# Kernel tuning notes

Measured on AMD Instinct MI355X. Metric: run time of the kernel, lower is better.

## Reference

```python
import jax, jax.numpy as jnp
import numpy as np

B, S, T, F, C = 32, 8, 1024, 128, 1
CLIP = 10.0

def setup_inputs() -> dict:
    key = jax.random.key(0)
    k1, k2 = jax.random.split(key)
    specs = jax.random.normal(k1, (B, S, T, F, C), dtype=jnp.float32)
    mask = jax.random.randint(k2, (B, S), 0, 2, dtype=jnp.int32)
    return {"specs": specs, "mask": mask}

def _axis_mask(key, dim, max_w, dtype):
    # Vectorized equivalent of one time/freq mask applied with prob 0.65 per (b,s) sample.
    k1, k2, k3 = jax.random.split(key, 3)
    width = jax.random.randint(k1, (B, S), 1, max_w + 1)              # [B,S]
    u = jax.random.uniform(k2, (B, S))
    start = jnp.floor(u * jnp.maximum(1, dim - width)).astype(jnp.int32)
    idx = jnp.arange(dim)                                             # [dim]
    zeroed = (idx[None, None, :] >= start[:, :, None]) & (idx[None, None, :] < (start + width)[:, :, None])
    apply = jax.random.uniform(k3, (B, S)) > 0.35
    m = jnp.where(apply[:, :, None], ~zeroed, True)                   # [B,S,dim] bool
    return m.astype(dtype)

def reference(specs, mask):
    # training=True, enabled=True path
    key = jax.random.key(42)
    kt1, kt2, kf1, kf2, kn_a, kn, ks_a, ks = jax.random.split(key, 8)
    dt = specs.dtype
    max_t = max(1, int(T * 0.12))
    max_f = max(1, int(F * 0.12))

    tm = _axis_mask(kt1, T, max_t, dt) * _axis_mask(kt2, T, max_t, dt)   # [B,S,T]
    fm = _axis_mask(kf1, F, max_f, dt) * _axis_mask(kf2, F, max_f, dt)   # [B,S,F]

    s = specs * tm[:, :, :, None, None] * fm[:, :, None, :, None]

    # additive noise with prob 0.55
    apply_n = (jax.random.uniform(kn_a, (B, S)) > 0.45).astype(dt)
    noise = 0.06 * jax.random.normal(kn, specs.shape, dtype=dt)
    s = s + noise * apply_n[:, :, None, None, None]

    # random scale with prob 0.5
    sc = jax.random.uniform(ks, (B, S), minval=0.85, maxval=1.15, dtype=dt)
    apply_s = jax.random.uniform(ks_a, (B, S)) > 0.5
    sc = jnp.where(apply_s, sc, jnp.ones_like(sc))
    s = s * sc[:, :, None, None, None]

    s = jnp.clip(s, -CLIP, CLIP)

    sensor_on = mask.astype(jnp.float32) > 0.5                           # [B,S]
    return jnp.where(sensor_on[:, :, None, None, None], s, specs)
```

## Files before the change

kernel.cpp:

```cpp
#include <hip/hip_runtime.h>
#include <stdint.h>

namespace {

constexpr int kB = 32, kS = 8, kT = 1024, kF = 128;
constexpr int kBS = kB * kS;
constexpr int kSlice = kT * kF;
constexpr uint32_t kSpanT = 122;
constexpr uint32_t kSpanF = 15;

struct BSParams {
  int ts1, te1, ts2, te2;
  int fs1, fe1, fs2, fe2;
  float scale;
  int apply_n;
  uint32_t kn0, kn1;
};

__device__ __forceinline__ uint32_t rotl32(uint32_t v, int d) {
  return (v << d) | (v >> (32 - d));
}

__device__ __forceinline__ void tf2x32(uint32_t k0, uint32_t k1, uint32_t x0, uint32_t x1,
                                       uint32_t& o0, uint32_t& o1) {
  const uint32_t ks0 = k0, ks1 = k1, ks2 = k0 ^ k1 ^ 0x1BD11BDAu;
  x0 += ks0; x1 += ks1;
  x0 += x1; x1 = rotl32(x1, 13); x1 ^= x0;
  x0 += x1; x1 = rotl32(x1, 15); x1 ^= x0;
  x0 += x1; x1 = rotl32(x1, 26); x1 ^= x0;
  x0 += x1; x1 = rotl32(x1, 6);  x1 ^= x0;
  x0 += ks1; x1 += ks2 + 1u;
  x0 += x1; x1 = rotl32(x1, 17); x1 ^= x0;
  x0 += x1; x1 = rotl32(x1, 29); x1 ^= x0;
  x0 += x1; x1 = rotl32(x1, 16); x1 ^= x0;
  x0 += x1; x1 = rotl32(x1, 24); x1 ^= x0;
  x0 += ks2; x1 += ks0 + 2u;
  x0 += x1; x1 = rotl32(x1, 13); x1 ^= x0;
  x0 += x1; x1 = rotl32(x1, 15); x1 ^= x0;
  x0 += x1; x1 = rotl32(x1, 26); x1 ^= x0;
  x0 += x1; x1 = rotl32(x1, 6);  x1 ^= x0;
  x0 += ks0; x1 += ks1 + 3u;
  x0 += x1; x1 = rotl32(x1, 17); x1 ^= x0;
  x0 += x1; x1 = rotl32(x1, 29); x1 ^= x0;
  x0 += x1; x1 = rotl32(x1, 16); x1 ^= x0;
  x0 += x1; x1 = rotl32(x1, 24); x1 ^= x0;
  x0 += ks1; x1 += ks2 + 4u;
  x0 += x1; x1 = rotl32(x1, 13); x1 ^= x0;
  x0 += x1; x1 = rotl32(x1, 15); x1 ^= x0;
  x0 += x1; x1 = rotl32(x1, 26); x1 ^= x0;
  x0 += x1; x1 = rotl32(x1, 6);  x1 ^= x0;
  x0 += ks2; x1 += ks0 + 5u;
  o0 = x0; o1 = x1;
}

__device__ __forceinline__ uint32_t bits32(uint32_t k0, uint32_t k1, uint32_t ctr) {
  uint32_t o0, o1;
  tf2x32(k0, k1, 0u, ctr, o0, o1);
  return o0 ^ o1;
}

__device__ __forceinline__ float u01(uint32_t bits) {
  return __uint_as_float(0x3f800000u | (bits >> 9)) - 1.0f;
}

__device__ __forceinline__ float erfinv_f(float x) {
  float w = -log1pf(-x * x);
  float p;
  if (w < 5.0f) {
    w -= 2.5f;
    p = 2.81022636e-08f;
    p = fmaf(p, w, 3.43273939e-07f);
    p = fmaf(p, w, -3.5233877e-06f);
    p = fmaf(p, w, -4.39150654e-06f);
    p = fmaf(p, w, 0.00021858087f);
    p = fmaf(p, w, -0.00125372503f);
    p = fmaf(p, w, -0.00417768164f);
    p = fmaf(p, w, 0.246640727f);
    p = fmaf(p, w, 1.50140941f);
  } else {
    w = sqrtf(w) - 3.0f;
    p = -0.000200214257f;
    p = fmaf(p, w, 0.000100950558f);
    p = fmaf(p, w, 0.00134934322f);
    p = fmaf(p, w, -0.00367342844f);
    p = fmaf(p, w, 0.00573950773f);
    p = fmaf(p, w, -0.0076224613f);
    p = fmaf(p, w, 0.00943887047f);
    p = fmaf(p, w, 1.00167406f);
    p = fmaf(p, w, 2.83297682f);
  }
  return p * x;
}

__device__ void axis_params(uint32_t K0, uint32_t K1, int dim, uint32_t span, uint32_t i,
                            int& start_out, int& end_out) {
  uint32_t k10, k11, k20, k21, k30, k31, a0, a1, b0, b1;
  tf2x32(K0, K1, 0u, 0u, k10, k11);
  tf2x32(K0, K1, 0u, 1u, k20, k21);
  tf2x32(K0, K1, 0u, 2u, k30, k31);
  tf2x32(k10, k11, 0u, 0u, a0, a1);
  tf2x32(k10, k11, 0u, 1u, b0, b1);
  uint32_t hi = bits32(a0, a1, i);
  uint32_t lo = bits32(b0, b1, i);
  uint32_t mult = 65536u % span;
  mult = (mult * mult) % span;
  uint32_t off = ((hi % span) * mult + (lo % span)) % span;
  int width = 1 + (int)off;
  float u = u01(bits32(k20, k21, i));
  int M = dim - width; if (M < 1) M = 1;
  int start = (int)floorf(u * (float)M);
  bool apply = u01(bits32(k30, k31, i)) > 0.35f;
  start_out = start;
  end_out = apply ? (start + width) : start;
}

__device__ BSParams compute_params(uint32_t i) {
  BSParams p;
  uint32_t w0, w1;
  tf2x32(0u, 42u, 0u, 0u, w0, w1); axis_params(w0, w1, kT, kSpanT, i, p.ts1, p.te1);
  tf2x32(0u, 42u, 0u, 1u, w0, w1); axis_params(w0, w1, kT, kSpanT, i, p.ts2, p.te2);
  tf2x32(0u, 42u, 0u, 2u, w0, w1); axis_params(w0, w1, kF, kSpanF, i, p.fs1, p.fe1);
  tf2x32(0u, 42u, 0u, 3u, w0, w1); axis_params(w0, w1, kF, kSpanF, i, p.fs2, p.fe2);
  tf2x32(0u, 42u, 0u, 4u, w0, w1);
  p.apply_n = (u01(bits32(w0, w1, i)) > 0.45f) ? 1 : 0;
  tf2x32(0u, 42u, 0u, 5u, p.kn0, p.kn1);
  tf2x32(0u, 42u, 0u, 6u, w0, w1);
  bool apply_s = u01(bits32(w0, w1, i)) > 0.5f;
  tf2x32(0u, 42u, 0u, 7u, w0, w1);
  float su = u01(bits32(w0, w1, i));
  float sc = fmaxf(0.85f, fmaf(su, 1.15f - 0.85f, 0.85f));
  p.scale = apply_s ? sc : 1.0f;
  return p;
}

__global__ void spec_params_kernel(BSParams* __restrict__ P) {
  uint32_t i = threadIdx.x;
  P[i] = compute_params(i);
}

template <bool USE_WS>
__global__ __launch_bounds__(256) void spec_main_kernel(const float* __restrict__ specs,
                                                        const int* __restrict__ mask,
                                                        float* __restrict__ out,
                                                        const BSParams* __restrict__ P) {
  const int bs = blockIdx.y;
  const int off = blockIdx.x * 2048 + threadIdx.x * 8;
  const long base = (long)bs * kSlice + off;
  const float4* in4 = reinterpret_cast<const float4*>(specs + base);
  float4 a = in4[0];
  float4 b = in4[1];
  float4* out4 = reinterpret_cast<float4*>(out + base);

  const bool on = (mask[bs] != 0);
  if (!on) {
    out4[0] = a; out4[1] = b;
    return;
  }

  BSParams p;
  if (USE_WS) p = P[bs]; else p = compute_params((uint32_t)bs);

  const int t = off >> 7;
  const int f0 = off & 127;
  const bool tm = !((t >= p.ts1) & (t < p.te1)) && !((t >= p.ts2) & (t < p.te2));

  const float LO = __int_as_float(0xBF7FFFFF);
  float v[8] = {a.x, a.y, a.z, a.w, b.x, b.y, b.z, b.w};

  if (p.apply_n) {
#pragma unroll
    for (int j = 0; j < 8; ++j) {
      const int f = f0 + j;
      const bool fm = !((f >= p.fs1) & (f < p.fe1)) && !((f >= p.fs2) & (f < p.fe2));
      float s = (tm && fm) ? v[j] : 0.0f;
      const uint32_t bits = bits32(p.kn0, p.kn1, (uint32_t)(base + j));
      float x = fmaxf(LO, u01(bits) * 2.0f + LO);
      s += 0.06f * (1.41421356f * erfinv_f(x));
      s *= p.scale;
      v[j] = fminf(10.0f, fmaxf(-10.0f, s));
    }
  } else {
#pragma unroll
    for (int j = 0; j < 8; ++j) {
      const int f = f0 + j;
      const bool fm = !((f >= p.fs1) & (f < p.fe1)) && !((f >= p.fs2) & (f < p.fe2));
      float s = (tm && fm) ? v[j] : 0.0f;
      s *= p.scale;
      v[j] = fminf(10.0f, fmaxf(-10.0f, s));
    }
  }

  out4[0] = make_float4(v[0], v[1], v[2], v[3]);
  out4[1] = make_float4(v[4], v[5], v[6], v[7]);
}

}

extern "C" void kernel_launch(void* const* d_in, const int* in_sizes, int n_in,
                              void* d_out, int out_size, void* d_ws, size_t ws_size,
                              hipStream_t stream) {
  const float* specs = (const float*)d_in[0];
  const int* mask = (const int*)d_in[1];
  float* out = (float*)d_out;

  dim3 grid(kSlice / 2048, kBS);
  dim3 block(256);

  if (ws_size >= sizeof(BSParams) * kBS) {
    BSParams* P = (BSParams*)d_ws;
    hipLaunchKernelGGL(spec_params_kernel, dim3(1), dim3(kBS), 0, stream, P);
    hipLaunchKernelGGL((spec_main_kernel<true>), grid, block, 0, stream, specs, mask, out, P);
  } else {
    hipLaunchKernelGGL((spec_main_kernel<false>), grid, block, 0, stream, specs, mask, out,
                       (const BSParams*)nullptr);
  }
}
```

Measured before the change: 62.76 us.

## Use fast erfinv, 16 elements per thread, bitmask freq masking, nontemporal stores

Replaces the erfinv with a branchless version built on hardware log and sqrt intrinsics. The tail branch becomes a crude linear fit in sqrt(w), so accuracy is lower for extreme noise samples. Each thread now handles 16 elements, and the frequency mask is precomputed as a bitmask. Outputs go through nontemporal stores. Together these cut per-element ALU work and divergence in the noise path, which is compute-heavy because of Threefry, at the risk of lower occupancy and numeric deviation in the tails.

```diff
diff --git a/kernel.cpp b/kernel.cpp
--- a/kernel.cpp
+++ b/kernel.cpp
@@ -8,6 +8,8 @@
 constexpr int kSlice = kT * kF;
 constexpr uint32_t kSpanT = 122;
 constexpr uint32_t kSpanF = 15;
+
+typedef float f32x4 __attribute__((ext_vector_type(4)));
 
 struct BSParams {
   int ts1, te1, ts2, te2;
@@ -63,32 +65,21 @@
   return __uint_as_float(0x3f800000u | (bits >> 9)) - 1.0f;
 }
 
-__device__ __forceinline__ float erfinv_f(float x) {
-  float w = -log1pf(-x * x);
-  float p;
-  if (w < 5.0f) {
-    w -= 2.5f;
-    p = 2.81022636e-08f;
-    p = fmaf(p, w, 3.43273939e-07f);
-    p = fmaf(p, w, -3.5233877e-06f);
-    p = fmaf(p, w, -4.39150654e-06f);
-    p = fmaf(p, w, 0.00021858087f);
-    p = fmaf(p, w, -0.00125372503f);
-    p = fmaf(p, w, -0.00417768164f);
-    p = fmaf(p, w, 0.246640727f);
-    p = fmaf(p, w, 1.50140941f);
-  } else {
-    w = sqrtf(w) - 3.0f;
-    p = -0.000200214257f;
-    p = fmaf(p, w, 0.000100950558f);
-    p = fmaf(p, w, 0.00134934322f);
-    p = fmaf(p, w, -0.00367342844f);
-    p = fmaf(p, w, 0.00573950773f);
-    p = fmaf(p, w, -0.0076224613f);
-    p = fmaf(p, w, 0.00943887047f);
-    p = fmaf(p, w, 1.00167406f);
-    p = fmaf(p, w, 2.83297682f);
-  }
+__device__ __forceinline__ float erfinv_fast(float x) {
+  float t = fmaf(-x, x, 1.0f);
+  float w = -0.69314718f * __builtin_amdgcn_logf(t);
+  float wm = w - 2.5f;
+  float p = 2.81022636e-08f;
+  p = fmaf(p, wm, 3.43273939e-07f);
+  p = fmaf(p, wm, -3.5233877e-06f);
+  p = fmaf(p, wm, -4.39150654e-06f);
+  p = fmaf(p, wm, 0.00021858087f);
+  p = fmaf(p, wm, -0.00125372503f);
+  p = fmaf(p, wm, -0.00417768164f);
+  p = fmaf(p, wm, 0.246640727f);
+  p = fmaf(p, wm, 1.50140941f);
+  float tail = fmaf(1.0003f, __builtin_amdgcn_sqrtf(w), -0.1623f);
+  p = (w < 5.0f) ? p : tail;
   return p * x;
 }
 
@@ -144,16 +135,17 @@
                                                         float* __restrict__ out,
                                                         const BSParams* __restrict__ P) {
   const int bs = blockIdx.y;
-  const int off = blockIdx.x * 2048 + threadIdx.x * 8;
+  const int off = blockIdx.x * 4096 + threadIdx.x * 16;
   const long base = (long)bs * kSlice + off;
-  const float4* in4 = reinterpret_cast<const float4*>(specs + base);
-  float4 a = in4[0];
-  float4 b = in4[1];
-  float4* out4 = reinterpret_cast<float4*>(out + base);
-
-  const bool on = (mask[bs] != 0);
-  if (!on) {
-    out4[0] = a; out4[1] = b;
+  const f32x4* in4 = reinterpret_cast<const f32x4*>(specs + base);
+  f32x4 a0 = in4[0], a1 = in4[1], a2 = in4[2], a3 = in4[3];
+  f32x4* out4 = reinterpret_cast<f32x4*>(out + base);
+
+  if (mask[bs] == 0) {
+    __builtin_nontemporal_store(a0, &out4[0]);
+    __builtin_nontemporal_store(a1, &out4[1]);
+    __builtin_nontemporal_store(a2, &out4[2]);
+    __builtin_nontemporal_store(a3, &out4[3]);
     return;
   }
 
@@ -164,34 +156,47 @@
   const int f0 = off & 127;
   const bool tm = !((t >= p.ts1) & (t < p.te1)) && !((t >= p.ts2) & (t < p.te2));
 
+  int lo1 = min(16, max(0, p.fs1 - f0)), hi1 = min(16, max(0, p.fe1 - f0));
+  int lo2 = min(16, max(0, p.fs2 - f0)), hi2 = min(16, max(0, p.fe2 - f0));
+  uint32_t z1 = ((1u << hi1) - 1u) & ~((1u << lo1) - 1u);
+  uint32_t z2 = ((1u << hi2) - 1u) & ~((1u << lo2) - 1u);
+  const uint32_t keep = tm ? (0xFFFFu & ~(z1 | z2)) : 0u;
+
+  float v[16] = {a0.x, a0.y, a0.z, a0.w, a1.x, a1.y, a1.z, a1.w,
+                 a2.x, a2.y, a2.z, a2.w, a3.x, a3.y, a3.z, a3.w};
+
   const float LO = __int_as_float(0xBF7FFFFF);
-  float v[8] = {a.x, a.y, a.z, a.w, b.x, b.y, b.z, b.w};
+  const float sc = p.scale;
 
   if (p.apply_n) {
+    const uint32_t c0 = (uint32_t)base;
 #pragma unroll
-    for (int j = 0; j < 8; ++j) {
-      const int f = f0 + j;
-      const bool fm = !((f >= p.fs1) & (f < p.fe1)) && !((f >= p.fs2) & (f < p.fe2));
-      float s = (tm && fm) ? v[j] : 0.0f;
-      const uint32_t bits = bits32(p.kn0, p.kn1, (uint32_t)(base + j));
-      float x = fmaxf(LO, u01(bits) * 2.0f + LO);
-      s += 0.06f * (1.41421356f * erfinv_f(x));
-      s *= p.scale;
+    for (int j = 0; j < 16; ++j) {
+      float s = (keep & (1u << j)) ? v[j] : 0.0f;
+      const uint32_t bits = bits32(p.kn0, p.kn1, c0 + (uint32_t)j);
+      float u1 = __uint_as_float(0x3f800000u | (bits >> 9));
+      float x = fmaxf(LO, fmaf(u1, 2.0f, -2.0f) + LO);
+      s = fmaf(0.08485281374f, erfinv_fast(x), s);
+      s *= sc;
       v[j] = fminf(10.0f, fmaxf(-10.0f, s));
     }
   } else {
 #pragma unroll
-    for (int j = 0; j < 8; ++j) {
-      const int f = f0 + j;
-      const bool fm = !((f >= p.fs1) & (f < p.fe1)) && !((f >= p.fs2) & (f < p.fe2));
-      float s = (tm && fm) ? v[j] : 0.0f;
-      s *= p.scale;
+    for (int j = 0; j < 16; ++j) {
+      float s = (keep & (1u << j)) ? v[j] : 0.0f;
+      s *= sc;
       v[j] = fminf(10.0f, fmaxf(-10.0f, s));
     }
   }
 
-  out4[0] = make_float4(v[0], v[1], v[2], v[3]);
-  out4[1] = make_float4(v[4], v[5], v[6], v[7]);
+  f32x4 r0 = {v[0], v[1], v[2], v[3]};
+  f32x4 r1 = {v[4], v[5], v[6], v[7]};
+  f32x4 r2 = {v[8], v[9], v[10], v[11]};
+  f32x4 r3 = {v[12], v[13], v[14], v[15]};
+  __builtin_nontemporal_store(r0, &out4[0]);
+  __builtin_nontemporal_store(r1, &out4[1]);
+  __builtin_nontemporal_store(r2, &out4[2]);
+  __builtin_nontemporal_store(r3, &out4[3]);
 }
 
 }
@@ -203,7 +208,7 @@
   const int* mask = (const int*)d_in[1];
   float* out = (float*)d_out;
 
-  dim3 grid(kSlice / 2048, kBS);
+  dim3 grid(kSlice / 4096, kBS);
   dim3 block(256);
 
   if (ws_size >= sizeof(BSParams) * kBS) {
```

New measurement: 100.8 us. 1.61x slower.
